# Optimization experiments

Hardware: AMD Instinct MI355X
Metric: run time of the kernel (lower is better)

Reference implementation:

```python
import jax, jax.numpy as jnp
import numpy as np

B, T, N, V, C, E = 64, 100, 25, 128, 128, 64
EPS = 1e-5


def setup_inputs() -> dict:
    key = jax.random.key(0)
    ks = jax.random.split(key, 6)
    x = jax.random.normal(ks[0], (B, T, N, V), jnp.float32)
    edge_index = jax.random.randint(ks[1], (2, E), 0, N, dtype=jnp.int64)
    W1 = jax.random.normal(ks[2], (V, C), jnp.float32) * (1.0 / np.sqrt(V))
    b1 = jnp.zeros((C,), jnp.float32)
    W2 = jax.random.normal(ks[3], (C, C), jnp.float32) * (1.0 / np.sqrt(C))
    b2 = jnp.zeros((C,), jnp.float32)
    gamma = jnp.ones((T,), jnp.float32)
    beta = jnp.zeros((T,), jnp.float32)
    return {"x": x, "edge_index": edge_index, "W1": W1, "b1": b1,
            "W2": W2, "b2": b2, "gamma": gamma, "beta": beta}


def _gcn_norm(edge_index, n):
    # GCNConv default: add self-loops, symmetric D^{-1/2} A_hat D^{-1/2} norm.
    loop = jnp.arange(n, dtype=edge_index.dtype)
    src = jnp.concatenate([edge_index[0], loop])  # [E + N]
    tgt = jnp.concatenate([edge_index[1], loop])
    deg = jnp.zeros((n,), jnp.float32).at[tgt].add(1.0)
    dis = jax.lax.rsqrt(deg)  # deg >= 1 due to self-loops
    return src, tgt, dis[src] * dis[tgt]


def _gcn_layer(h, W, b, src, tgt, norm):
    # h: [G, N, Cin] -> [G, N, Cout]; linear then gather-scale-scatter aggregate.
    h = jnp.einsum('gnc,cd->gnd', h, W)
    msg = h[:, src, :] * norm[None, :, None]          # [G, E+N, Cout]
    out = jnp.zeros_like(h).at[:, tgt, :].add(msg)    # scatter-add to targets
    return out + b


def reference(x, edge_index, W1, b1, W2, b2, gamma, beta):
    Bv, Tv, Nv, Vv = x.shape
    h = x.reshape(Bv * Tv, Nv, Vv)  # B*T independent graphs, shared edge_index
    src, tgt, norm = _gcn_norm(edge_index, Nv)
    h = _gcn_layer(h, W1, b1, src, tgt, norm)
    h = _gcn_layer(h, W2, b2, src, tgt, norm)
    y = h.reshape(Bv, Tv, Nv, -1)
    # BatchNorm2d(T) in training mode: batch stats over (B, N, C) per T-channel.
    mean = y.mean(axis=(0, 2, 3), keepdims=True)
    var = y.var(axis=(0, 2, 3), keepdims=True)  # biased, matches torch normalization
    y = (y - mean) * jax.lax.rsqrt(var + EPS)
    y = y * gamma[None, :, None, None] + beta[None, :, None, None]
    return jax.nn.relu(y)
```

## Files before the change

kernel.cpp:

```cpp
#include <hip/hip_runtime.h>

#define T_DIM   100
#define N_NODES 25
#define C_DIM   128
#define B_DIM   64
#define G_TOTAL 6400
#define GNV     3200
#define CNT_PER_T 204800.0f

#define WS_A2   0
#define WS_RS1  640
#define WS_BW   768
#define WS_SUM  1024
#define WS_SSQ  1152
#define WS_W12T 2048

typedef __attribute__((ext_vector_type(8))) short short8;
typedef __attribute__((ext_vector_type(4))) float f32x4;

__device__ __forceinline__ unsigned short f2bf(float f) {
  unsigned int u = __float_as_uint(f);
  u += 0x7FFFu + ((u >> 16) & 1u);
  return (unsigned short)(u >> 16);
}

__global__ void k_prep(const int* __restrict__ edge, float* __restrict__ wsf) {
  __shared__ float sA[N_NODES][N_NODES];
  __shared__ float sdeg[N_NODES];
  __shared__ float sdis[N_NODES];
  const int tid = threadIdx.x;

  if (tid < N_NODES) sdeg[tid] = 0.f;
  for (int j = tid; j < N_NODES * N_NODES; j += 256) ((float*)sA)[j] = 0.f;
  __syncthreads();
  if (tid < 64) atomicAdd(&sdeg[edge[64 + tid]], 1.f);
  __syncthreads();
  if (tid < N_NODES) sdis[tid] = rsqrtf(sdeg[tid] + 1.f);
  __syncthreads();
  if (tid < 64) {
    int s = edge[tid], tg = edge[64 + tid];
    atomicAdd(&sA[tg][s], sdis[s] * sdis[tg]);
  }
  __syncthreads();
  if (tid < N_NODES) atomicAdd(&sA[tid][tid], sdis[tid] * sdis[tid]);
  __syncthreads();
  for (int j = tid; j < N_NODES * N_NODES; j += 256) {
    int n = j / N_NODES, m = j - n * N_NODES;
    float acc = 0.f;
    for (int k = 0; k < N_NODES; k++) acc = fmaf(sA[n][k], sA[k][m], acc);
    wsf[WS_A2 + j] = acc;
  }
  if (tid < N_NODES) {
    float rs = 0.f;
    for (int m = 0; m < N_NODES; m++) rs += sA[tid][m];
    wsf[WS_RS1 + tid] = rs;
  }
  if (tid < T_DIM) { wsf[WS_SUM + tid] = 0.f; wsf[WS_SSQ + tid] = 0.f; }
}

__global__ void k_wprep(const float* __restrict__ W1, const float* __restrict__ W2,
                        const float* __restrict__ b1, float* __restrict__ wsf) {
  int j = blockIdx.x * 256 + threadIdx.x;
  int c = j & 127, v = j >> 7;
  float acc = 0.f;
#pragma unroll 8
  for (int u = 0; u < 128; u++) acc = fmaf(W1[v * 128 + u], W2[u * 128 + c], acc);
  ((unsigned short*)(wsf + WS_W12T))[c * 128 + v] = f2bf(acc);
  if (j < 128) {
    float a2 = 0.f;
    for (int u = 0; u < 128; u++) a2 = fmaf(W2[u * 128 + j], b1[u], a2);
    wsf[WS_BW + j] = a2;
  }
}

__global__ __launch_bounds__(256) void k_main(const float* __restrict__ x,
                                              const float* __restrict__ b2,
                                              const float* __restrict__ wsc,
                                              float* __restrict__ stats,
                                              float* __restrict__ out) {
  __shared__ __align__(16) unsigned short XA[112 * 128];
  __shared__ __align__(16) unsigned short WT[128 * 128];
  __shared__ float rs1[32];
  __shared__ float red[8];
  const int tid = threadIdx.x;
  const int bid = blockIdx.x;
  const int t = bid % T_DIM;
  const int bq = bid / T_DIM;

  {
    const uint4* wg = (const uint4*)(wsc + WS_W12T);
    uint4* wl = (uint4*)WT;
    for (int j = tid; j < 2048; j += 256) {
      int row = j >> 4, cc = j & 15;
      wl[(row << 4) | (cc ^ (row & 15))] = wg[j];
    }
  }
  if (tid < N_NODES) rs1[tid] = wsc[WS_RS1 + tid];
  for (int j = tid; j < 12 * 128; j += 256)
    XA[(100 + (j >> 7)) * 128 + (j & 127)] = 0;

  {
    const int v = tid & 127;
    const int gl0 = tid >> 7;
    const float* A2 = wsc + WS_A2;
    const int g0 = (bq * 4 + gl0) * T_DIM + t;
    const float* xp0 = x + g0 * GNV + v;
    const float* xp1 = xp0 + 2 * T_DIM * GNV;
    float x0[25], x1[25];
#pragma unroll
    for (int m = 0; m < 25; m++) { x0[m] = xp0[m * 128]; x1[m] = xp1[m * 128]; }
    for (int n = 0; n < 25; n++) {
      float a0 = 0.f, a1 = 0.f;
#pragma unroll
      for (int m = 0; m < 25; m++) {
        float w = A2[n * 25 + m];
        a0 = fmaf(w, x0[m], a0);
        a1 = fmaf(w, x1[m], a1);
      }
      int r0 = gl0 * 25 + n, r1 = r0 + 50;
      XA[r0 * 128 + (v ^ ((r0 & 15) << 3))] = f2bf(a0);
      XA[r1 * 128 + (v ^ ((r1 & 15) << 3))] = f2bf(a1);
    }
  }
  __syncthreads();

  const int wv = tid >> 6, lane = tid & 63, quad = lane >> 4, l16 = lane & 15;
  f32x4 acc[7][2];
#pragma unroll
  for (int mt = 0; mt < 7; mt++)
#pragma unroll
    for (int nt = 0; nt < 2; nt++)
#pragma unroll
      for (int r = 0; r < 4; r++) acc[mt][nt][r] = 0.f;

#pragma unroll
  for (int ks = 0; ks < 4; ks++) {
    const int cc = (ks << 2) | quad;
    short8 bfr[2];
#pragma unroll
    for (int nt = 0; nt < 2; nt++) {
      int brow = wv * 32 + nt * 16 + l16;
      bfr[nt] = *(const short8*)&WT[brow * 128 + ((cc ^ (brow & 15)) << 3)];
    }
#pragma unroll
    for (int mt = 0; mt < 7; mt++) {
      int arow = mt * 16 + l16;
      short8 afr = *(const short8*)&XA[arow * 128 + ((cc ^ (arow & 15)) << 3)];
#pragma unroll
      for (int nt = 0; nt < 2; nt++)
        acc[mt][nt] = __builtin_amdgcn_mfma_f32_16x16x32_bf16(afr, bfr[nt], acc[mt][nt], 0, 0, 0);
    }
  }

  const int c0i = wv * 32 + l16;
  const float bw0 = wsc[WS_BW + c0i], bw1 = wsc[WS_BW + c0i + 16];
  const float bb0 = b2[c0i], bb1 = b2[c0i + 16];
  float sum = 0.f, ssq = 0.f;
#pragma unroll
  for (int mt = 0; mt < 7; mt++) {
#pragma unroll
    for (int r = 0; r < 4; r++) {
      int row = mt * 16 + quad * 4 + r;
      if (row < 100) {
        int gl = row / 25;
        int n = row - gl * 25;
        float rsn = rs1[n];
        int g = (bq * 4 + gl) * T_DIM + t;
        int ob = g * GNV + n * 128 + c0i;
        float v0 = acc[mt][0][r] + rsn * bw0 + bb0;
        float v1 = acc[mt][1][r] + rsn * bw1 + bb1;
        out[ob] = v0;
        out[ob + 16] = v1;
        sum += v0 + v1;
        ssq += v0 * v0 + v1 * v1;
      }
    }
  }
#pragma unroll
  for (int off = 32; off > 0; off >>= 1) {
    sum += __shfl_down(sum, off, 64);
    ssq += __shfl_down(ssq, off, 64);
  }
  if (lane == 0) { red[wv] = sum; red[4 + wv] = ssq; }
  __syncthreads();
  if (tid == 0) {
    atomicAdd(&stats[t], red[0] + red[1] + red[2] + red[3]);
    atomicAdd(&stats[128 + t], red[4] + red[5] + red[6] + red[7]);
  }
}

__global__ __launch_bounds__(256) void k_norm(float* __restrict__ out,
                                              const float* __restrict__ stats,
                                              const float* __restrict__ gamma,
                                              const float* __restrict__ beta) {
  int i4 = blockIdx.x * 256 + threadIdx.x;
  int base = i4 * 4;
  int t = (base / GNV) % T_DIM;
  float s = stats[t], q = stats[128 + t];
  const float inv = 1.f / CNT_PER_T;
  float mean = s * inv;
  float var = fmaf(q, inv, -mean * mean);
  float rstd = rsqrtf(var + 1e-5f);
  float g = gamma[t] * rstd;
  float b = fmaf(-mean, g, beta[t]);
  float4 h = *(const float4*)(out + base);
  h.x = fmaxf(fmaf(h.x, g, b), 0.f);
  h.y = fmaxf(fmaf(h.y, g, b), 0.f);
  h.z = fmaxf(fmaf(h.z, g, b), 0.f);
  h.w = fmaxf(fmaf(h.w, g, b), 0.f);
  *(float4*)(out + base) = h;
}

extern "C" void kernel_launch(void* const* d_in, const int* in_sizes, int n_in,
                              void* d_out, int out_size, void* d_ws, size_t ws_size,
                              hipStream_t stream) {
  const float* x     = (const float*)d_in[0];
  const int*   edge  = (const int*)d_in[1];
  const float* W1    = (const float*)d_in[2];
  const float* b1    = (const float*)d_in[3];
  const float* W2    = (const float*)d_in[4];
  const float* b2    = (const float*)d_in[5];
  const float* gamma = (const float*)d_in[6];
  const float* beta  = (const float*)d_in[7];
  float* out = (float*)d_out;
  float* wsf = (float*)d_ws;

  k_prep<<<1, 256, 0, stream>>>(edge, wsf);
  k_wprep<<<64, 256, 0, stream>>>(W1, W2, b1, wsf);
  k_main<<<G_TOTAL / 4, 256, 0, stream>>>(x, b2, wsf, wsf + WS_SUM, out);
  k_norm<<<(B_DIM * T_DIM * GNV) / 4 / 256, 256, 0, stream>>>(out, wsf + WS_SUM, gamma, beta);
}
```

Before: 223.4 us.

## Load combined weight fragments into registers directly and batch norm-pass loads per thread

In the main kernel, the bf16 combined-weight tile is no longer staged through 32 KB of LDS. Each wave now loads its B fragments for all k-steps straight from global memory into registers, and launch bounds request 4 blocks per CU. Less shared memory per block should allow higher occupancy and drops the LDS staging copy, at the cost of more VGPRs and redundant global weight reads across blocks. The normalisation kernel now has each thread process four strided float4 chunks, with loads issued before stores to raise memory-level parallelism and cut the block count.

```diff
diff --git a/kernel.cpp b/kernel.cpp
--- a/kernel.cpp
+++ b/kernel.cpp
@@ -73,28 +73,20 @@
   }
 }
 
-__global__ __launch_bounds__(256) void k_main(const float* __restrict__ x,
-                                              const float* __restrict__ b2,
-                                              const float* __restrict__ wsc,
-                                              float* __restrict__ stats,
-                                              float* __restrict__ out) {
+__global__ __launch_bounds__(256, 4) void k_main(const float* __restrict__ x,
+                                                 const float* __restrict__ b2,
+                                                 const float* __restrict__ wsc,
+                                                 float* __restrict__ stats,
+                                                 float* __restrict__ out) {
   __shared__ __align__(16) unsigned short XA[112 * 128];
-  __shared__ __align__(16) unsigned short WT[128 * 128];
   __shared__ float rs1[32];
   __shared__ float red[8];
   const int tid = threadIdx.x;
   const int bid = blockIdx.x;
   const int t = bid % T_DIM;
   const int bq = bid / T_DIM;
-
-  {
-    const uint4* wg = (const uint4*)(wsc + WS_W12T);
-    uint4* wl = (uint4*)WT;
-    for (int j = tid; j < 2048; j += 256) {
-      int row = j >> 4, cc = j & 15;
-      wl[(row << 4) | (cc ^ (row & 15))] = wg[j];
-    }
-  }
+  const int wv = tid >> 6, lane = tid & 63, quad = lane >> 4, l16 = lane & 15;
+
   if (tid < N_NODES) rs1[tid] = wsc[WS_RS1 + tid];
   for (int j = tid; j < 12 * 128; j += 256)
     XA[(100 + (j >> 7)) * 128 + (j & 127)] = 0;
@@ -122,9 +114,19 @@
       XA[r1 * 128 + (v ^ ((r1 & 15) << 3))] = f2bf(a1);
     }
   }
-  __syncthreads();
-
-  const int wv = tid >> 6, lane = tid & 63, quad = lane >> 4, l16 = lane & 15;
+
+  short8 bfr[2][4];
+  {
+    const unsigned short* Wg = (const unsigned short*)(wsc + WS_W12T);
+#pragma unroll
+    for (int nt = 0; nt < 2; nt++) {
+      const short8* rp = (const short8*)&Wg[(wv * 32 + nt * 16 + l16) * 128];
+#pragma unroll
+      for (int ks = 0; ks < 4; ks++) bfr[nt][ks] = rp[(ks << 2) | quad];
+    }
+  }
+  __syncthreads();
+
   f32x4 acc[7][2];
 #pragma unroll
   for (int mt = 0; mt < 7; mt++)
@@ -136,19 +138,13 @@
 #pragma unroll
   for (int ks = 0; ks < 4; ks++) {
     const int cc = (ks << 2) | quad;
-    short8 bfr[2];
-#pragma unroll
-    for (int nt = 0; nt < 2; nt++) {
-      int brow = wv * 32 + nt * 16 + l16;
-      bfr[nt] = *(const short8*)&WT[brow * 128 + ((cc ^ (brow & 15)) << 3)];
-    }
 #pragma unroll
     for (int mt = 0; mt < 7; mt++) {
       int arow = mt * 16 + l16;
       short8 afr = *(const short8*)&XA[arow * 128 + ((cc ^ (arow & 15)) << 3)];
 #pragma unroll
       for (int nt = 0; nt < 2; nt++)
-        acc[mt][nt] = __builtin_amdgcn_mfma_f32_16x16x32_bf16(afr, bfr[nt], acc[mt][nt], 0, 0, 0);
+        acc[mt][nt] = __builtin_amdgcn_mfma_f32_16x16x32_bf16(afr, bfr[nt][ks], acc[mt][nt], 0, 0, 0);
     }
   }
 
@@ -189,26 +185,39 @@
   }
 }
 
+#define NORM_T4   5120000
+#define NORM_STR  1280000
 __global__ __launch_bounds__(256) void k_norm(float* __restrict__ out,
                                               const float* __restrict__ stats,
                                               const float* __restrict__ gamma,
                                               const float* __restrict__ beta) {
-  int i4 = blockIdx.x * 256 + threadIdx.x;
-  int base = i4 * 4;
-  int t = (base / GNV) % T_DIM;
-  float s = stats[t], q = stats[128 + t];
+  const int i0 = blockIdx.x * 256 + threadIdx.x;
   const float inv = 1.f / CNT_PER_T;
-  float mean = s * inv;
-  float var = fmaf(q, inv, -mean * mean);
-  float rstd = rsqrtf(var + 1e-5f);
-  float g = gamma[t] * rstd;
-  float b = fmaf(-mean, g, beta[t]);
-  float4 h = *(const float4*)(out + base);
-  h.x = fmaxf(fmaf(h.x, g, b), 0.f);
-  h.y = fmaxf(fmaf(h.y, g, b), 0.f);
-  h.z = fmaxf(fmaf(h.z, g, b), 0.f);
-  h.w = fmaxf(fmaf(h.w, g, b), 0.f);
-  *(float4*)(out + base) = h;
+  float4 h[4];
+  float g[4], bb[4];
+  int base[4];
+#pragma unroll
+  for (int k = 0; k < 4; k++) {
+    int i4 = i0 + k * NORM_STR;
+    base[k] = i4 * 4;
+    int t = (base[k] / GNV) % T_DIM;
+    float s = stats[t], q = stats[128 + t];
+    float mean = s * inv;
+    float var = fmaf(q, inv, -mean * mean);
+    float rstd = rsqrtf(var + 1e-5f);
+    g[k] = gamma[t] * rstd;
+    bb[k] = fmaf(-mean, g[k], beta[t]);
+    h[k] = *(const float4*)(out + base[k]);
+  }
+#pragma unroll
+  for (int k = 0; k < 4; k++) {
+    float4 v = h[k];
+    v.x = fmaxf(fmaf(v.x, g[k], bb[k]), 0.f);
+    v.y = fmaxf(fmaf(v.y, g[k], bb[k]), 0.f);
+    v.z = fmaxf(fmaf(v.z, g[k], bb[k]), 0.f);
+    v.w = fmaxf(fmaf(v.w, g[k], bb[k]), 0.f);
+    *(float4*)(out + base[k]) = v;
+  }
 }
 
 extern "C" void kernel_launch(void* const* d_in, const int* in_sizes, int n_in,
@@ -228,5 +237,5 @@
   k_prep<<<1, 256, 0, stream>>>(edge, wsf);
   k_wprep<<<64, 256, 0, stream>>>(W1, W2, b1, wsf);
   k_main<<<G_TOTAL / 4, 256, 0, stream>>>(x, b2, wsf, wsf + WS_SUM, out);
-  k_norm<<<(B_DIM * T_DIM * GNV) / 4 / 256, 256, 0, stream>>>(out, wsf + WS_SUM, gamma, beta);
-}
+  k_norm<<<NORM_STR / 256, 256, 0, stream>>>(out, wsf + WS_SUM, gamma, beta);
+}
```

After: 215.0 us. -3.8%, faster.
